# Optimization experiments

Hardware: AMD Instinct MI355X
Metric: run time of the kernel (lower is better)

The kernel has to match this reference:

```python
import jax, jax.numpy as jnp
import numpy as np

NC = 80          # num_classes
REG_MAX = 16
TOPK = 10
IMG = 640
STRIDES = (8, 16, 32)
EPS = 1e-9


def make_anchors(shapes, strides):
    pts, strs = [], []
    for (h, w), s in zip(shapes, strides):
        sx = jnp.arange(w, dtype=jnp.float32)  # grid_cell_offset = 0.0
        sy = jnp.arange(h, dtype=jnp.float32)
        gy, gx = jnp.meshgrid(sy, sx, indexing='ij')
        pts.append(jnp.stack([gx, gy], -1).reshape(-1, 2))
        strs.append(jnp.full((h * w, 1), float(s), dtype=jnp.float32))
    return jnp.concatenate(pts, 0), jnp.concatenate(strs, 0)  # [A,2], [A,1]


def ciou(box1, box2, eps=1e-7):
    # boxes are xyxy, broadcastable; returns CIoU with last dim squeezed
    b1x1, b1y1, b1x2, b1y2 = jnp.split(box1, 4, -1)
    b2x1, b2y1, b2x2, b2y2 = jnp.split(box2, 4, -1)
    w1, h1 = b1x2 - b1x1, b1y2 - b1y1
    w2, h2 = b2x2 - b2x1, b2y2 - b2y1
    inter = (jnp.clip(jnp.minimum(b1x2, b2x2) - jnp.maximum(b1x1, b2x1), 0.0)
             * jnp.clip(jnp.minimum(b1y2, b2y2) - jnp.maximum(b1y1, b2y1), 0.0))
    union = w1 * h1 + w2 * h2 - inter + eps
    iou = inter / union
    cw = jnp.maximum(b1x2, b2x2) - jnp.minimum(b1x1, b2x1)
    ch = jnp.maximum(b1y2, b2y2) - jnp.minimum(b1y1, b2y1)
    c2 = cw ** 2 + ch ** 2 + eps
    rho2 = ((b2x1 + b2x2 - b1x1 - b1x2) ** 2 + (b2y1 + b2y2 - b1y1 - b1y2) ** 2) / 4.0
    v = (4.0 / np.pi ** 2) * (jnp.arctan(w2 / (h2 + eps)) - jnp.arctan(w1 / (h1 + eps))) ** 2
    alpha = jax.lax.stop_gradient(v / (v - iou + (1.0 + eps)))
    return (iou - (rho2 / c2 + v * alpha))[..., 0]


def bbox_decode(anchor_points, pred_distri):
    # distribution-focal decode: softmax over REG_MAX bins, expectation, dist2bbox
    B, A, _ = pred_distri.shape
    pd = pred_distri.reshape(B, A, 4, REG_MAX)
    proj = jnp.arange(REG_MAX, dtype=jnp.float32)
    dist = jnp.einsum('bacr,r->bac', jax.nn.softmax(pd, -1), proj)  # [B,A,4] ltrb
    lt, rb = dist[..., :2], dist[..., 2:]
    return jnp.concatenate([anchor_points - lt, anchor_points + rb], -1)  # xyxy


def assigner(pd_scores, pd_bboxes, anc_points, gt_labels, gt_bboxes, mask_gt,
             alpha=0.5, beta=6.0):
    # pd_scores [B,A,C] (sigmoid), pd_bboxes [B,A,4], gt_* [B,M,...], mask_gt [B,M,1]
    B, A, C = pd_scores.shape
    M = gt_bboxes.shape[1]
    mask_gt = mask_gt.astype(jnp.float32)
    # anchors whose center lies inside each gt box
    lt = anc_points[None, None, :, :] - gt_bboxes[:, :, None, :2]   # [B,M,A,2]
    rb = gt_bboxes[:, :, None, 2:] - anc_points[None, None, :, :]
    mask_in_gts = (jnp.minimum(lt.min(-1), rb.min(-1)) > EPS).astype(jnp.float32)  # [B,M,A]
    mask = mask_in_gts * mask_gt
    # class score of each anchor at the gt's label
    sc = jnp.take_along_axis(pd_scores[:, None, :, :],
                             gt_labels[:, :, None, None].astype(jnp.int32), axis=-1)[..., 0]  # [B,M,A]
    overlaps = jnp.clip(ciou(gt_bboxes[:, :, None, :], pd_bboxes[:, None, :, :]), 0.0) * mask
    bbox_scores = sc * mask
    align_metric = (bbox_scores ** alpha) * (overlaps ** beta)  # [B,M,A]
    # top-k candidates per gt
    _, idxs = jax.lax.top_k(align_metric, TOPK)                 # [B,M,K]
    valid = jnp.broadcast_to(mask_gt > 0, (B, M, TOPK))
    idxs = jnp.where(valid, idxs, 0)
    cnt = jnp.zeros((B * M, A), jnp.float32).at[
        jnp.arange(B * M)[:, None], idxs.reshape(B * M, TOPK)
    ].add(valid.reshape(B * M, TOPK).astype(jnp.float32)).reshape(B, M, A)
    mask_topk = jnp.where(cnt > 1, 0.0, cnt)
    mask_pos = mask_topk * mask_in_gts * mask_gt               # [B,M,A]
    # resolve anchors assigned to multiple gts by max overlap
    fg = mask_pos.sum(1)                                       # [B,A]
    multi = fg[:, None, :] > 1
    is_max = jax.nn.one_hot(overlaps.argmax(1), M, dtype=jnp.float32).transpose(0, 2, 1)
    mask_pos = jnp.where(multi, is_max, mask_pos)
    fg_mask = mask_pos.sum(1)                                  # [B,A]
    tgt_idx = mask_pos.argmax(1)                               # [B,A]
    # gather targets
    flat = tgt_idx + jnp.arange(B)[:, None] * M
    t_labels = jnp.clip(gt_labels.reshape(-1)[flat], 0)        # [B,A]
    t_bboxes = gt_bboxes.reshape(-1, 4)[flat]                  # [B,A,4]
    t_scores = jax.nn.one_hot(t_labels, C, dtype=jnp.float32) * (fg_mask[..., None] > 0)
    # normalize scores by aligned metric
    am = align_metric * mask_pos
    pos_am = am.max(-1, keepdims=True)                         # [B,M,1]
    pos_ov = (overlaps * mask_pos).max(-1, keepdims=True)      # [B,M,1]
    norm = (am * pos_ov / (pos_am + EPS)).max(1)[..., None]    # [B,A,1]
    return t_bboxes, t_scores * norm, fg_mask > 0


def setup_inputs() -> dict:
    key = jax.random.key(0)
    ks = jax.random.split(key, 9)
    B, M = 16, 32
    inp = {
        'cls0': jax.random.normal(ks[0], (B, NC, 80, 80), jnp.float32),
        'cls1': jax.random.normal(ks[1], (B, NC, 40, 40), jnp.float32),
        'cls2': jax.random.normal(ks[2], (B, NC, 20, 20), jnp.float32),
        'reg0': jax.random.normal(ks[3], (B, 4 * REG_MAX, 80, 80), jnp.float32),
        'reg1': jax.random.normal(ks[4], (B, 4 * REG_MAX, 40, 40), jnp.float32),
        'reg2': jax.random.normal(ks[5], (B, 4 * REG_MAX, 20, 20), jnp.float32),
    }
    cxy = jax.random.uniform(ks[6], (B, M, 2), minval=0.1, maxval=0.9)
    wh = jax.random.uniform(ks[7], (B, M, 2), minval=0.02, maxval=0.25)
    inp['boxes'] = jnp.concatenate([cxy, wh], -1)  # normalized cxcywh
    inp['labels'] = jax.random.randint(ks[8], (B, M), 0, NC)
    return inp


def reference(cls0, cls1, cls2, reg0, reg1, reg2, boxes, labels):
    cls_out, reg_out = [cls0, cls1, cls2], [reg0, reg1, reg2]
    B = cls0.shape[0]
    anc, stride_t = make_anchors([r.shape[2:] for r in reg_out], STRIDES)
    pred_scores = jnp.concatenate(
        [c.transpose(0, 2, 3, 1).reshape(B, -1, NC) for c in cls_out], 1)        # [B,A,C]
    pred_distri = jnp.concatenate(
        [r.transpose(0, 2, 3, 1).reshape(B, -1, 4 * REG_MAX) for r in reg_out], 1)
    # gt2xyxy: normalized cxcywh -> pixel xyxy
    cx, cy, w, h = jnp.split(boxes, 4, -1)
    gt_bboxes = jnp.concatenate([(cx - w / 2) * IMG, (cy - h / 2) * IMG,
                                 (cx + w / 2) * IMG, (cy + h / 2) * IMG], -1)
    mask_gt = gt_bboxes.sum(2, keepdims=True) > 0.0
    pred_bboxes = bbox_decode(anc, pred_distri)                                   # anchor units
    sg = jax.lax.stop_gradient
    t_bboxes, t_scores, fg_mask = assigner(
        sg(jax.nn.sigmoid(pred_scores)), sg(pred_bboxes) * stride_t,
        anc * stride_t, labels, gt_bboxes, mask_gt)
    tss = jnp.maximum(t_scores.sum(), 1.0)
    # classification BCE-with-logits
    x, t = pred_scores, t_scores
    bce = jnp.maximum(x, 0.0) - x * t + jnp.log1p(jnp.exp(-jnp.abs(x)))
    l_cls = bce.sum() / tss
    # bbox CIoU loss
    t_bboxes = t_bboxes / stride_t
    weight = t_scores.sum(-1) * fg_mask                                           # [B,A]
    iou = ciou(pred_bboxes, t_bboxes)
    l_iou = ((1.0 - iou) * weight).sum() / tss
    # DFL loss
    tltrb = jnp.clip(jnp.concatenate([anc - t_bboxes[..., :2],
                                      t_bboxes[..., 2:] - anc], -1),
                     0.0, REG_MAX - 1 - 0.01)                                     # [B,A,4]
    logp = jax.nn.log_softmax(pred_distri.reshape(B, -1, 4, REG_MAX), -1)
    tl = jnp.floor(tltrb).astype(jnp.int32)
    wl = (tl + 1).astype(jnp.float32) - tltrb
    lp_tl = jnp.take_along_axis(logp, tl[..., None], -1)[..., 0]
    lp_tr = jnp.take_along_axis(logp, (tl + 1)[..., None], -1)[..., 0]
    dfl = (-(lp_tl * wl + lp_tr * (1.0 - wl))).mean(-1)                           # [B,A]
    l_dfl = (dfl * weight).sum() / tss
    loss = jnp.stack([0.5 * l_cls, 7.5 * l_iou, 1.5 * l_dfl])
    return loss.sum(), loss
```

## Files before the change

kernel.cpp:

```cpp
#include <hip/hip_runtime.h>

#define NB 16
#define NM 32
#define NA 8400
#define NCC 80
#define NREG 64
#define A0 6400
#define A1 1600
#define A2 400
#define CAP 768

#define TILES_PER_B 34
#define DEC_BLKS (NB * TILES_PER_B)
#define BCE_BLKS 2048
#define PRE_GRID (DEC_BLKS + BCE_BLKS)
#define PL_GRID 525


__device__ __forceinline__ void anch(int a, float& ax, float& ay, float& s, int& lvl, int& p) {
  if (a < A0)            { lvl = 0; p = a;          s = 8.f;  ax = (float)(p % 80); ay = (float)(p / 80); }
  else if (a < A0 + A1)  { lvl = 1; p = a - A0;     s = 16.f; ax = (float)(p % 40); ay = (float)(p / 40); }
  else                   { lvl = 2; p = a - A0 - A1; s = 32.f; ax = (float)(p % 20); ay = (float)(p / 20); }
}

__device__ __forceinline__ float cls_at(const float* c0, const float* c1, const float* c2,
                                        int b, int ch, int a) {
  if (a < A0)           return c0[((size_t)(b * NCC + ch)) * A0 + a];
  if (a < A0 + A1)      return c1[((size_t)(b * NCC + ch)) * A1 + (a - A0)];
  return c2[((size_t)(b * NCC + ch)) * A2 + (a - A0 - A1)];
}

__device__ __forceinline__ float reg_at(const float* r0, const float* r1, const float* r2,
                                        int b, int ch, int lvl, int p) {
  if (lvl == 0) return r0[((size_t)(b * NREG + ch)) * A0 + p];
  if (lvl == 1) return r1[((size_t)(b * NREG + ch)) * A1 + p];
  return r2[((size_t)(b * NREG + ch)) * A2 + p];
}

__device__ __forceinline__ void gtbox(const float* boxes, int b, int m,
                                      float& x1, float& y1, float& x2, float& y2, bool& valid) {
  const float* q = boxes + ((size_t)(b * NM + m)) * 4;
  float cx = q[0], cy = q[1], w = q[2], h = q[3];
  x1 = (cx - w * 0.5f) * 640.f; y1 = (cy - h * 0.5f) * 640.f;
  x2 = (cx + w * 0.5f) * 640.f; y2 = (cy + h * 0.5f) * 640.f;
  valid = (x1 + y1 + x2 + y2) > 0.f;
}

__device__ __forceinline__ float ciou_f(float b1x1, float b1y1, float b1x2, float b1y2,
                                        float b2x1, float b2y1, float b2x2, float b2y2) {
  const float eps = 1e-7f;
  float w1 = b1x2 - b1x1, h1 = b1y2 - b1y1;
  float w2 = b2x2 - b2x1, h2 = b2y2 - b2y1;
  float iw = fmaxf(fminf(b1x2, b2x2) - fmaxf(b1x1, b2x1), 0.f);
  float ih = fmaxf(fminf(b1y2, b2y2) - fmaxf(b1y1, b2y1), 0.f);
  float inter = iw * ih;
  float uni = w1 * h1 + w2 * h2 - inter + eps;
  float iou = inter / uni;
  float cw = fmaxf(b1x2, b2x2) - fminf(b1x1, b2x1);
  float ch = fmaxf(b1y2, b2y2) - fminf(b1y1, b2y1);
  float c2 = cw * cw + ch * ch + eps;
  float dx = b2x1 + b2x2 - b1x1 - b1x2;
  float dy = b2y1 + b2y2 - b1y1 - b1y2;
  float rho2 = (dx * dx + dy * dy) * 0.25f;
  float at = atanf(w2 / (h2 + eps)) - atanf(w1 / (h1 + eps));
  float v = 0.4052847345693511f * at * at;
  float alpha = v / (v - iou + (1.0f + eps));
  return iou - (rho2 / c2 + v * alpha);
}

__device__ __forceinline__ float align_of(float sc, float o) {
  float o2 = o * o, o4 = o2 * o2;
  return sqrtf(sc) * (o2 * o4);
}

__device__ __forceinline__ float softplus_fast(float x) {
  float e = __expf(-fabsf(x));
  return fmaxf(x, 0.f) + __logf(1.f + e);
}


__global__ __launch_bounds__(256) void k_pre3(
    const float* r0, const float* r1, const float* r2,
    const float* c0, const float* c1, const float* c2,
    float4* bb4, float4* mls4, int* fgcnt, int* msum,
    unsigned* pos_am, unsigned* pos_ov, double* gt_acc, double* bce_part) {
  __shared__ __align__(8) float lds[32 * 256];
  const int tid = threadIdx.x;

  if (blockIdx.x < DEC_BLKS) {
    const int d = blockIdx.x;
    const int b = d / TILES_PER_B, u = d % TILES_PER_B;
    int lvl, tile;
    if (u < 25)      { lvl = 0; tile = u; }
    else if (u < 32) { lvl = 1; tile = u - 25; }
    else             { lvl = 2; tile = u - 32; }
    const int HW   = (lvl == 0) ? A0 : (lvl == 1 ? A1 : A2);
    const int W    = (lvl == 0) ? 80 : (lvl == 1 ? 40 : 20);
    const int loff = (lvl == 0) ? 0  : (lvl == 1 ? A0 : A0 + A1);
    const float* rg = (lvl == 0) ? r0 : (lvl == 1 ? r1 : r2);
    const int base_p = tile * 256;
    const int valid  = min(256, HW - base_p);
    const float* src = rg + (size_t)b * NREG * HW + base_p;

    float dist[4], mlv[4];
#pragma unroll
    for (int ph = 0; ph < 2; ++ph) {
      for (int ch = 0; ch < 32; ++ch) {
        if (tid < valid)
          lds[ch * 256 + tid] = src[(size_t)(ph * 32 + ch) * HW + tid];
      }
      __syncthreads();
      if (tid < valid) {
#pragma unroll
        for (int sh = 0; sh < 2; ++sh) {
          const float* col = &lds[(sh * 16) * 256 + tid];
          float mx = col[0];
#pragma unroll
          for (int r = 1; r < 16; ++r) mx = fmaxf(mx, col[r * 256]);
          float se = 0.f, ws = 0.f;
#pragma unroll
          for (int r = 0; r < 16; ++r) {
            float e = __expf(col[r * 256] - mx);
            se += e; ws += e * (float)r;
          }
          dist[ph * 2 + sh] = ws / se;
          mlv[ph * 2 + sh]  = mx + __logf(se);
        }
      }
      __syncthreads();
    }
    if (tid < valid) {
      int p = base_p + tid;
      float ax = (float)(p % W), ay = (float)(p / W);
      int t = b * NA + loff + p;
      bb4[t]  = make_float4(ax - dist[0], ay - dist[1], ax + dist[2], ay + dist[3]);
      mls4[t] = make_float4(mlv[0], mlv[1], mlv[2], mlv[3]);
    }
  } else {
    const int bce_blk = blockIdx.x - DEC_BLKS;
    const int gz = bce_blk * 256 + tid;
    if (gz < NB * NA) { fgcnt[gz] = 0; msum[gz] = 0; }
    if (gz < NB * NM) { pos_am[gz] = 0u; pos_ov[gz] = 0u; }
    if (gz < NB * NM * 4) gt_acc[gz] = 0.0;

    const size_t N0 = (size_t)NB * NCC * A0 / 4;
    const size_t N1 = (size_t)NB * NCC * A1 / 4;
    const size_t N2 = (size_t)NB * NCC * A2 / 4;
    const size_t NT = N0 + N1 + N2;
    const float4* f0 = (const float4*)c0;
    const float4* f1 = (const float4*)c1;
    const float4* f2 = (const float4*)c2;
    const size_t i0 = (size_t)bce_blk * 256 + tid;
    const size_t stride = (size_t)BCE_BLKS * 256;
    float s0 = 0.f, s1 = 0.f;
    for (size_t i = i0; i < NT; i += stride) {
      float4 v;
      if (i < N0) v = f0[i];
      else if (i < N0 + N1) v = f1[i - N0];
      else v = f2[i - N0 - N1];
      s0 += softplus_fast(v.x) + softplus_fast(v.z);
      s1 += softplus_fast(v.y) + softplus_fast(v.w);
    }
    double* sred = (double*)lds;
    sred[tid] = (double)(s0 + s1);
    __syncthreads();
    for (int off = 128; off; off >>= 1) {
      if (tid < off) sred[tid] += sred[tid + off];
      __syncthreads();
    }
    if (tid == 0) bce_part[bce_blk] = sred[0];
  }
}


__global__ __launch_bounds__(256) void k_assign(
    const float* boxes, const int* labels, const float4* bb,
    const float* c0, const float* c1, const float* c2,
    int* fgcnt, int* msum) {
  __shared__ float sv[CAP];
  __shared__ int   si[CAP];
  __shared__ int   s_n;
  const int bm = blockIdx.x;
  const int b = bm / NM, m = bm % NM;
  const int tid = threadIdx.x;
  const int lane = tid & 63;

  float gx1, gy1, gx2, gy2; bool valid;
  gtbox(boxes, b, m, gx1, gy1, gx2, gy2, valid);
  if (!valid) return;
  int lbl = labels[bm]; if (lbl < 0) lbl = 0; if (lbl >= NCC) lbl = NCC - 1;
  if (tid == 0) s_n = 0;
  __syncthreads();

  const int   Ws[3]   = {80, 40, 20};
  const float ss[3]   = {8.f, 16.f, 32.f};
  const int   loff[3] = {0, A0, A0 + A1};
  int rx0[3], ry0[3], rw[3], bc[3];
  int total = 0;
  for (int l = 0; l < 3; ++l) {
    float s = ss[l]; int W = Ws[l];
    int ax0 = (int)floorf((gx1 + 1e-9f) / s);
    int ax1 = (int)ceilf((gx2 - 1e-9f) / s);
    int ay0 = (int)floorf((gy1 + 1e-9f) / s);
    int ay1 = (int)ceilf((gy2 - 1e-9f) / s);
    ax0 = max(ax0, 0); ay0 = max(ay0, 0);
    ax1 = min(ax1, W - 1); ay1 = min(ay1, W - 1);
    rx0[l] = ax0; ry0[l] = ay0;
    rw[l] = max(0, ax1 - ax0 + 1);
    int rhl = max(0, ay1 - ay0 + 1);
    bc[l] = total;
    total += rw[l] * rhl;
  }
  int iters = (total + 255) >> 8;
  for (int it = 0; it < iters; ++it) {
    int idx = it * 256 + tid;
    bool pred = false; float am = 0.f; int a = 0;
    if (idx < total) {
      int l = (idx >= bc[2]) ? 2 : ((idx >= bc[1]) ? 1 : 0);
      int r = idx - bc[l];
      int iy = r / rw[l], ix = r - iy * rw[l];
      int axg = rx0[l] + ix, ayg = ry0[l] + iy;
      a = loff[l] + ayg * Ws[l] + axg;
      float s = ss[l];
      float axp = (float)axg * s, ayp = (float)ayg * s;
      float mn = fminf(fminf(axp - gx1, ayp - gy1), fminf(gx2 - axp, gy2 - ayp));
      if (mn > 1e-9f) {
        pred = true;
        float4 pb = bb[(size_t)b * NA + a];
        float c = ciou_f(gx1, gy1, gx2, gy2, pb.x * s, pb.y * s, pb.z * s, pb.w * s);
        float o = fmaxf(c, 0.f);
        float x = cls_at(c0, c1, c2, b, lbl, a);
        float sc = 1.f / (1.f + expf(-x));
        am = align_of(sc, o);
      }
    }
    unsigned long long mask = __ballot(pred);
    if (mask) {
      int nact = __popcll(mask);
      int leader = __ffsll(mask) - 1;
      int basec = 0;
      if (lane == leader) basec = atomicAdd(&s_n, nact);
      basec = __shfl(basec, leader);
      if (pred) {
        int off = basec + __popcll(mask & ((1ull << lane) - 1ull));
        if (off < CAP) { sv[off] = am; si[off] = a; }
      }
    }
  }
  __syncthreads();
  int n = s_n; if (n > CAP) n = CAP;
  if (n == 0) return;
  if (tid >= 64) return;

  float v[12]; int ix[12];
#pragma unroll
  for (int k = 0; k < 12; ++k) {
    int j = k * 64 + tid;
    bool in = (j < n);
    v[k]  = in ? sv[j] : -2.f;
    ix[k] = in ? si[j] : (1 << 30);
  }
  int cnt = 0;
#pragma unroll
  for (int k = 0; k < 12; ++k) cnt += (v[k] > 0.f) ? 1 : 0;
  for (int o = 32; o; o >>= 1) cnt += __shfl_xor(cnt, o);
  int npos = cnt;

  if (npos > 10) {
    for (int p = 0; p < 10; ++p) {
      float bv = -1.f; int bi = 1 << 30;
#pragma unroll
      for (int k = 0; k < 12; ++k) {
        if (v[k] > bv || (v[k] == bv && ix[k] < bi)) { bv = v[k]; bi = ix[k]; }
      }
      for (int o = 32; o; o >>= 1) {
        float wv = __shfl_xor(bv, o); int wi = __shfl_xor(bi, o);
        if (wv > bv || (wv == bv && wi < bi)) { bv = wv; bi = wi; }
      }
#pragma unroll
      for (int k = 0; k < 12; ++k) if (ix[k] == bi) v[k] = -1.f;
      if (tid == 0) {
        atomicAdd(&fgcnt[(size_t)b * NA + bi], 1);
        atomicAdd(&msum[(size_t)b * NA + bi], m);
      }
    }
  } else {
#pragma unroll
    for (int k = 0; k < 12; ++k) {
      if (v[k] > 0.f) {
        atomicAdd(&fgcnt[(size_t)b * NA + ix[k]], 1);
        atomicAdd(&msum[(size_t)b * NA + ix[k]], m);
      }
    }
    int need = 10 - npos;
    for (int j = tid; j < n; j += 64) {
      if (sv[j] == 0.f) {
        int i = si[j];
        if (i < 10) {
          int pb = 0;
          for (int q = 0; q < n; ++q) pb += (sv[q] > 0.f && si[q] < i) ? 1 : 0;
          if (i - pb < need) {
            atomicAdd(&fgcnt[(size_t)b * NA + i], 1);
            atomicAdd(&msum[(size_t)b * NA + i], m);
          }
        }
      }
    }
  }
}


__global__ __launch_bounds__(256) void k_rp(
    const float* boxes, const int* labels,
    const float4* bb, const float4* mls,
    const float* c0, const float* c1, const float* c2,
    const float* r0, const float* r1, const float* r2,
    const int* fgcnt, const int* msum,
    unsigned* pos_am, unsigned* pos_ov, double* gt_acc) {
  int t = blockIdx.x * 256 + threadIdx.x;
  if (t >= NB * NA) return;
  int fg = fgcnt[t];
  if (fg == 0) return;
  int b = t / NA, a = t % NA;
  float ax, ay, s; int lvl, p;
  anch(a, ax, ay, s, lvl, p);
  float axp = ax * s, ayp = ay * s;
  float4 pb = bb[t];
  float px1 = pb.x * s, py1 = pb.y * s, px2 = pb.z * s, py2 = pb.w * s;
  int asn; float o;
  if (fg == 1) {
    asn = msum[t];
    float gx1, gy1, gx2, gy2; bool valid;
    gtbox(boxes, b, asn, gx1, gy1, gx2, gy2, valid);
    o = fmaxf(ciou_f(gx1, gy1, gx2, gy2, px1, py1, px2, py2), 0.f);
  } else {
    float bv = -1e30f; int bi = 0;
    for (int m = 0; m < NM; ++m) {
      float gx1, gy1, gx2, gy2; bool valid;
      gtbox(boxes, b, m, gx1, gy1, gx2, gy2, valid);
      float om = 0.f;
      if (valid) {
        float mn = fminf(fminf(axp - gx1, ayp - gy1), fminf(gx2 - axp, gy2 - ayp));
        if (mn > 1e-9f)
          om = fmaxf(ciou_f(gx1, gy1, gx2, gy2, px1, py1, px2, py2), 0.f);
      }
      if (om > bv) { bv = om; bi = m; }
    }
    asn = bi; o = bv;
  }
  if (o <= 0.f) return;
  int g = b * NM + asn;
  int lbl = labels[g]; if (lbl < 0) lbl = 0; if (lbl >= NCC) lbl = NCC - 1;
  float x = cls_at(c0, c1, c2, b, lbl, a);
  float sc = 1.f / (1.f + expf(-x));
  float am = align_of(sc, o);
  atomicMax(&pos_am[g], __float_as_uint(am));
  atomicMax(&pos_ov[g], __float_as_uint(o));
  if (am <= 0.f) return;

  float gx1, gy1, gx2, gy2; bool valid;
  gtbox(boxes, b, asn, gx1, gy1, gx2, gy2, valid);
  float inv_s = 1.f / s;
  float tx1 = gx1 * inv_s, ty1 = gy1 * inv_s, tx2 = gx2 * inv_s, ty2 = gy2 * inv_s;
  float iou = ciou_f(pb.x, pb.y, pb.z, pb.w, tx1, ty1, tx2, ty2);
  float4 ml = mls[t];
  float tgt[4] = { ax - tx1, ay - ty1, tx2 - ax, ty2 - ay };
  float mlv[4] = { ml.x, ml.y, ml.z, ml.w };
  float dfl = 0.f;
  for (int sd = 0; sd < 4; ++sd) {
    float tv = fminf(fmaxf(tgt[sd], 0.f), 14.99f);
    float tlf = floorf(tv);
    int tl = (int)tlf;
    float wl = (tlf + 1.f) - tv;
    float xtl = reg_at(r0, r1, r2, b, sd * 16 + tl,     lvl, p);
    float xtr = reg_at(r0, r1, r2, b, sd * 16 + tl + 1, lvl, p);
    dfl += -((xtl - mlv[sd]) * wl + (xtr - mlv[sd]) * (1.f - wl));
  }
  dfl *= 0.25f;
  atomicAdd(&gt_acc[g * 4 + 0], (double)am);
  atomicAdd(&gt_acc[g * 4 + 1], (double)(am * x));
  atomicAdd(&gt_acc[g * 4 + 2], (double)(am * (1.f - iou)));
  atomicAdd(&gt_acc[g * 4 + 3], (double)(am * dfl));
}


__global__ __launch_bounds__(256) void k_final(const double* bce_part, const double* gt_acc,
                                               const unsigned* pos_am, const unsigned* pos_ov,
                                               float* out) {
  const int tid = threadIdx.x;
  double tss = 0.0, sx = 0.0, siou = 0.0, sdfl = 0.0, bce = 0.0;
  for (int g = tid; g < NB * NM; g += 256) {
    float pam = __uint_as_float(pos_am[g]);
    float pov = __uint_as_float(pos_ov[g]);
    double sc = (double)pov / ((double)pam + 1e-9);
    tss  += gt_acc[g * 4 + 0] * sc;
    sx   += gt_acc[g * 4 + 1] * sc;
    siou += gt_acc[g * 4 + 2] * sc;
    sdfl += gt_acc[g * 4 + 3] * sc;
  }
  for (int i = tid; i < BCE_BLKS; i += 256) bce += bce_part[i];
  __shared__ double sred[256];
  double vals[5] = { tss, sx, siou, sdfl, bce };
  double tot[5];
  for (int q = 0; q < 5; ++q) {
    sred[tid] = vals[q];
    __syncthreads();
    for (int off = 128; off; off >>= 1) {
      if (tid < off) sred[tid] += sred[tid + off];
      __syncthreads();
    }
    tot[q] = sred[0];
    __syncthreads();
  }
  if (tid == 0) {
    double t = tot[0]; if (t < 1.0) t = 1.0;
    double l0 = 0.5 * (tot[4] - tot[1]) / t;
    double l1 = 7.5 * tot[2] / t;
    double l2 = 1.5 * tot[3] / t;
    out[0] = (float)(l0 + l1 + l2);
    out[1] = (float)l0;
    out[2] = (float)l1;
    out[3] = (float)l2;
  }
}


extern "C" void kernel_launch(void* const* d_in, const int* in_sizes, int n_in,
                              void* d_out, int out_size, void* d_ws, size_t ws_size,
                              hipStream_t stream) {
  (void)in_sizes; (void)n_in; (void)out_size; (void)ws_size;
  const float* cls0  = (const float*)d_in[0];
  const float* cls1  = (const float*)d_in[1];
  const float* cls2  = (const float*)d_in[2];
  const float* reg0  = (const float*)d_in[3];
  const float* reg1  = (const float*)d_in[4];
  const float* reg2  = (const float*)d_in[5];
  const float* boxes = (const float*)d_in[6];
  const int*   labels = (const int*)d_in[7];
  float* out = (float*)d_out;

  const size_t BA = (size_t)NB * NA;
  const int    BM = NB * NM;

  char* wsb = (char*)d_ws;
  double*   bce_part = (double*)wsb;
  double*   gt_acc   = bce_part + BCE_BLKS;
  unsigned* pos_am   = (unsigned*)(gt_acc + (size_t)BM * 4);
  unsigned* pos_ov   = pos_am + BM;
  int*      fgcnt    = (int*)(pos_ov + BM);
  int*      msum     = fgcnt + BA;
  float*    bbp      = (float*)(msum + BA);
  float*    mlsp     = bbp + BA * 4;

  float4* bb  = (float4*)bbp;
  float4* mls = (float4*)mlsp;

  k_pre3<<<PRE_GRID, 256, 0, stream>>>(reg0, reg1, reg2, cls0, cls1, cls2,
                                       bb, mls, fgcnt, msum, pos_am, pos_ov,
                                       gt_acc, bce_part);
  k_assign<<<BM, 256, 0, stream>>>(boxes, labels, (const float4*)bb,
                                   cls0, cls1, cls2, fgcnt, msum);
  k_rp<<<PL_GRID, 256, 0, stream>>>(boxes, labels, (const float4*)bb, (const float4*)mls,
                                    cls0, cls1, cls2, reg0, reg1, reg2,
                                    fgcnt, msum, pos_am, pos_ov, gt_acc);
  k_final<<<1, 256, 0, stream>>>(bce_part, gt_acc, pos_am, pos_ov, out);
}
```

Measured before the change: 64.58 us.

## Regroup kernels: BCE with assignment, fold final reduction into last block

The decode kernel now only decodes boxes and zeroes the workspace. The class-BCE reduction moves into the assignment kernel's grid, so its many blocks run alongside the 512 assignment blocks instead of alongside decode. The separate final-reduction kernel is removed: the per-anchor kernel ends with an atomic completion counter, and the last block to finish does the global reduction. This cuts one launch and improves GPU fill during assignment. The cost is a global atomic per block plus atomic reads to see other blocks' results.

```diff
diff --git a/kernel.cpp b/kernel.cpp
--- a/kernel.cpp
+++ b/kernel.cpp
@@ -12,8 +12,9 @@
 
 #define TILES_PER_B 34
 #define DEC_BLKS (NB * TILES_PER_B)
+#define ASN_BLKS (NB * NM)
 #define BCE_BLKS 2048
-#define PRE_GRID (DEC_BLKS + BCE_BLKS)
+#define MID_GRID (ASN_BLKS + BCE_BLKS)
 #define PL_GRID 525
 
 
@@ -79,70 +80,81 @@
 }
 
 
-__global__ __launch_bounds__(256) void k_pre3(
+__global__ __launch_bounds__(256) void k_dec(
     const float* r0, const float* r1, const float* r2,
+    float4* bb4, float4* mls4, int* fgcnt, int* msum,
+    unsigned* pos_am, unsigned* pos_ov, double* gt_acc, int* done_ctr) {
+  __shared__ float lds[32 * 256];
+  const int tid = threadIdx.x;
+  const int g = blockIdx.x * 256 + tid;
+  if (g < NB * NA) { fgcnt[g] = 0; msum[g] = 0; }
+  if (g < NB * NM) { pos_am[g] = 0u; pos_ov[g] = 0u; }
+  if (g < NB * NM * 4) gt_acc[g] = 0.0;
+  if (g == 0) *done_ctr = 0;
+
+  const int d = blockIdx.x;
+  const int b = d / TILES_PER_B, u = d % TILES_PER_B;
+  int lvl, tile;
+  if (u < 25)      { lvl = 0; tile = u; }
+  else if (u < 32) { lvl = 1; tile = u - 25; }
+  else             { lvl = 2; tile = u - 32; }
+  const int HW   = (lvl == 0) ? A0 : (lvl == 1 ? A1 : A2);
+  const int W    = (lvl == 0) ? 80 : (lvl == 1 ? 40 : 20);
+  const int loff = (lvl == 0) ? 0  : (lvl == 1 ? A0 : A0 + A1);
+  const float* rg = (lvl == 0) ? r0 : (lvl == 1 ? r1 : r2);
+  const int base_p = tile * 256;
+  const int valid  = min(256, HW - base_p);
+  const float* src = rg + (size_t)b * NREG * HW + base_p;
+
+  float dist[4], mlv[4];
+#pragma unroll
+  for (int ph = 0; ph < 2; ++ph) {
+    for (int ch = 0; ch < 32; ++ch) {
+      if (tid < valid)
+        lds[ch * 256 + tid] = src[(size_t)(ph * 32 + ch) * HW + tid];
+    }
+    __syncthreads();
+    if (tid < valid) {
+#pragma unroll
+      for (int sh = 0; sh < 2; ++sh) {
+        const float* col = &lds[(sh * 16) * 256 + tid];
+        float mx = col[0];
+#pragma unroll
+        for (int r = 1; r < 16; ++r) mx = fmaxf(mx, col[r * 256]);
+        float se = 0.f, ws = 0.f;
+#pragma unroll
+        for (int r = 0; r < 16; ++r) {
+          float e = __expf(col[r * 256] - mx);
+          se += e; ws += e * (float)r;
+        }
+        dist[ph * 2 + sh] = ws / se;
+        mlv[ph * 2 + sh]  = mx + __logf(se);
+      }
+    }
+    __syncthreads();
+  }
+  if (tid < valid) {
+    int p = base_p + tid;
+    float ax = (float)(p % W), ay = (float)(p / W);
+    int t = b * NA + loff + p;
+    bb4[t]  = make_float4(ax - dist[0], ay - dist[1], ax + dist[2], ay + dist[3]);
+    mls4[t] = make_float4(mlv[0], mlv[1], mlv[2], mlv[3]);
+  }
+}
+
+
+__global__ __launch_bounds__(256) void k_mid(
+    const float* boxes, const int* labels, const float4* bb,
     const float* c0, const float* c1, const float* c2,
-    float4* bb4, float4* mls4, int* fgcnt, int* msum,
-    unsigned* pos_am, unsigned* pos_ov, double* gt_acc, double* bce_part) {
-  __shared__ __align__(8) float lds[32 * 256];
+    int* fgcnt, int* msum, double* bce_part) {
+  __shared__ float sv[CAP];
+  __shared__ int   si[CAP];
+  __shared__ int   s_n;
+  __shared__ double sred[256];
   const int tid = threadIdx.x;
 
-  if (blockIdx.x < DEC_BLKS) {
-    const int d = blockIdx.x;
-    const int b = d / TILES_PER_B, u = d % TILES_PER_B;
-    int lvl, tile;
-    if (u < 25)      { lvl = 0; tile = u; }
-    else if (u < 32) { lvl = 1; tile = u - 25; }
-    else             { lvl = 2; tile = u - 32; }
-    const int HW   = (lvl == 0) ? A0 : (lvl == 1 ? A1 : A2);
-    const int W    = (lvl == 0) ? 80 : (lvl == 1 ? 40 : 20);
-    const int loff = (lvl == 0) ? 0  : (lvl == 1 ? A0 : A0 + A1);
-    const float* rg = (lvl == 0) ? r0 : (lvl == 1 ? r1 : r2);
-    const int base_p = tile * 256;
-    const int valid  = min(256, HW - base_p);
-    const float* src = rg + (size_t)b * NREG * HW + base_p;
-
-    float dist[4], mlv[4];
-#pragma unroll
-    for (int ph = 0; ph < 2; ++ph) {
-      for (int ch = 0; ch < 32; ++ch) {
-        if (tid < valid)
-          lds[ch * 256 + tid] = src[(size_t)(ph * 32 + ch) * HW + tid];
-      }
-      __syncthreads();
-      if (tid < valid) {
-#pragma unroll
-        for (int sh = 0; sh < 2; ++sh) {
-          const float* col = &lds[(sh * 16) * 256 + tid];
-          float mx = col[0];
-#pragma unroll
-          for (int r = 1; r < 16; ++r) mx = fmaxf(mx, col[r * 256]);
-          float se = 0.f, ws = 0.f;
-#pragma unroll
-          for (int r = 0; r < 16; ++r) {
-            float e = __expf(col[r * 256] - mx);
-            se += e; ws += e * (float)r;
-          }
-          dist[ph * 2 + sh] = ws / se;
-          mlv[ph * 2 + sh]  = mx + __logf(se);
-        }
-      }
-      __syncthreads();
-    }
-    if (tid < valid) {
-      int p = base_p + tid;
-      float ax = (float)(p % W), ay = (float)(p / W);
-      int t = b * NA + loff + p;
-      bb4[t]  = make_float4(ax - dist[0], ay - dist[1], ax + dist[2], ay + dist[3]);
-      mls4[t] = make_float4(mlv[0], mlv[1], mlv[2], mlv[3]);
-    }
-  } else {
-    const int bce_blk = blockIdx.x - DEC_BLKS;
-    const int gz = bce_blk * 256 + tid;
-    if (gz < NB * NA) { fgcnt[gz] = 0; msum[gz] = 0; }
-    if (gz < NB * NM) { pos_am[gz] = 0u; pos_ov[gz] = 0u; }
-    if (gz < NB * NM * 4) gt_acc[gz] = 0.0;
-
+  if (blockIdx.x >= ASN_BLKS) {
+    const int bce_blk = blockIdx.x - ASN_BLKS;
     const size_t N0 = (size_t)NB * NCC * A0 / 4;
     const size_t N1 = (size_t)NB * NCC * A1 / 4;
     const size_t N2 = (size_t)NB * NCC * A2 / 4;
@@ -161,7 +173,6 @@
       s0 += softplus_fast(v.x) + softplus_fast(v.z);
       s1 += softplus_fast(v.y) + softplus_fast(v.w);
     }
-    double* sred = (double*)lds;
     sred[tid] = (double)(s0 + s1);
     __syncthreads();
     for (int off = 128; off; off >>= 1) {
@@ -169,20 +180,11 @@
       __syncthreads();
     }
     if (tid == 0) bce_part[bce_blk] = sred[0];
-  }
-}
-
-
-__global__ __launch_bounds__(256) void k_assign(
-    const float* boxes, const int* labels, const float4* bb,
-    const float* c0, const float* c1, const float* c2,
-    int* fgcnt, int* msum) {
-  __shared__ float sv[CAP];
-  __shared__ int   si[CAP];
-  __shared__ int   s_n;
+    return;
+  }
+
   const int bm = blockIdx.x;
   const int b = bm / NM, m = bm % NM;
-  const int tid = threadIdx.x;
   const int lane = tid & 63;
 
   float gx1, gy1, gx2, gy2; bool valid;
@@ -310,93 +312,99 @@
 }
 
 
-__global__ __launch_bounds__(256) void k_rp(
+__global__ __launch_bounds__(256) void k_rpf(
     const float* boxes, const int* labels,
     const float4* bb, const float4* mls,
     const float* c0, const float* c1, const float* c2,
     const float* r0, const float* r1, const float* r2,
     const int* fgcnt, const int* msum,
-    unsigned* pos_am, unsigned* pos_ov, double* gt_acc) {
-  int t = blockIdx.x * 256 + threadIdx.x;
-  if (t >= NB * NA) return;
+    unsigned* pos_am, unsigned* pos_ov, double* gt_acc,
+    int* done_ctr, const double* bce_part, float* out) {
+  const int tid = threadIdx.x;
+  const int t = blockIdx.x * 256 + tid;
   int fg = fgcnt[t];
-  if (fg == 0) return;
-  int b = t / NA, a = t % NA;
-  float ax, ay, s; int lvl, p;
-  anch(a, ax, ay, s, lvl, p);
-  float axp = ax * s, ayp = ay * s;
-  float4 pb = bb[t];
-  float px1 = pb.x * s, py1 = pb.y * s, px2 = pb.z * s, py2 = pb.w * s;
-  int asn; float o;
-  if (fg == 1) {
-    asn = msum[t];
-    float gx1, gy1, gx2, gy2; bool valid;
-    gtbox(boxes, b, asn, gx1, gy1, gx2, gy2, valid);
-    o = fmaxf(ciou_f(gx1, gy1, gx2, gy2, px1, py1, px2, py2), 0.f);
-  } else {
-    float bv = -1e30f; int bi = 0;
-    for (int m = 0; m < NM; ++m) {
+  if (fg > 0) {
+    int b = t / NA, a = t % NA;
+    float ax, ay, s; int lvl, p;
+    anch(a, ax, ay, s, lvl, p);
+    float axp = ax * s, ayp = ay * s;
+    float4 pb = bb[t];
+    float px1 = pb.x * s, py1 = pb.y * s, px2 = pb.z * s, py2 = pb.w * s;
+    int asn; float o;
+    if (fg == 1) {
+      asn = msum[t];
       float gx1, gy1, gx2, gy2; bool valid;
-      gtbox(boxes, b, m, gx1, gy1, gx2, gy2, valid);
-      float om = 0.f;
-      if (valid) {
-        float mn = fminf(fminf(axp - gx1, ayp - gy1), fminf(gx2 - axp, gy2 - ayp));
-        if (mn > 1e-9f)
-          om = fmaxf(ciou_f(gx1, gy1, gx2, gy2, px1, py1, px2, py2), 0.f);
-      }
-      if (om > bv) { bv = om; bi = m; }
-    }
-    asn = bi; o = bv;
-  }
-  if (o <= 0.f) return;
-  int g = b * NM + asn;
-  int lbl = labels[g]; if (lbl < 0) lbl = 0; if (lbl >= NCC) lbl = NCC - 1;
-  float x = cls_at(c0, c1, c2, b, lbl, a);
-  float sc = 1.f / (1.f + expf(-x));
-  float am = align_of(sc, o);
-  atomicMax(&pos_am[g], __float_as_uint(am));
-  atomicMax(&pos_ov[g], __float_as_uint(o));
-  if (am <= 0.f) return;
-
-  float gx1, gy1, gx2, gy2; bool valid;
-  gtbox(boxes, b, asn, gx1, gy1, gx2, gy2, valid);
-  float inv_s = 1.f / s;
-  float tx1 = gx1 * inv_s, ty1 = gy1 * inv_s, tx2 = gx2 * inv_s, ty2 = gy2 * inv_s;
-  float iou = ciou_f(pb.x, pb.y, pb.z, pb.w, tx1, ty1, tx2, ty2);
-  float4 ml = mls[t];
-  float tgt[4] = { ax - tx1, ay - ty1, tx2 - ax, ty2 - ay };
-  float mlv[4] = { ml.x, ml.y, ml.z, ml.w };
-  float dfl = 0.f;
-  for (int sd = 0; sd < 4; ++sd) {
-    float tv = fminf(fmaxf(tgt[sd], 0.f), 14.99f);
-    float tlf = floorf(tv);
-    int tl = (int)tlf;
-    float wl = (tlf + 1.f) - tv;
-    float xtl = reg_at(r0, r1, r2, b, sd * 16 + tl,     lvl, p);
-    float xtr = reg_at(r0, r1, r2, b, sd * 16 + tl + 1, lvl, p);
-    dfl += -((xtl - mlv[sd]) * wl + (xtr - mlv[sd]) * (1.f - wl));
-  }
-  dfl *= 0.25f;
-  atomicAdd(&gt_acc[g * 4 + 0], (double)am);
-  atomicAdd(&gt_acc[g * 4 + 1], (double)(am * x));
-  atomicAdd(&gt_acc[g * 4 + 2], (double)(am * (1.f - iou)));
-  atomicAdd(&gt_acc[g * 4 + 3], (double)(am * dfl));
-}
-
-
-__global__ __launch_bounds__(256) void k_final(const double* bce_part, const double* gt_acc,
-                                               const unsigned* pos_am, const unsigned* pos_ov,
-                                               float* out) {
-  const int tid = threadIdx.x;
+      gtbox(boxes, b, asn, gx1, gy1, gx2, gy2, valid);
+      o = fmaxf(ciou_f(gx1, gy1, gx2, gy2, px1, py1, px2, py2), 0.f);
+    } else {
+      float bv = -1e30f; int bi = 0;
+      for (int m = 0; m < NM; ++m) {
+        float gx1, gy1, gx2, gy2; bool valid;
+        gtbox(boxes, b, m, gx1, gy1, gx2, gy2, valid);
+        float om = 0.f;
+        if (valid) {
+          float mn = fminf(fminf(axp - gx1, ayp - gy1), fminf(gx2 - axp, gy2 - ayp));
+          if (mn > 1e-9f)
+            om = fmaxf(ciou_f(gx1, gy1, gx2, gy2, px1, py1, px2, py2), 0.f);
+        }
+        if (om > bv) { bv = om; bi = m; }
+      }
+      asn = bi; o = bv;
+    }
+    if (o > 0.f) {
+      int g = b * NM + asn;
+      int lbl = labels[g]; if (lbl < 0) lbl = 0; if (lbl >= NCC) lbl = NCC - 1;
+      float x = cls_at(c0, c1, c2, b, lbl, a);
+      float sc = 1.f / (1.f + expf(-x));
+      float am = align_of(sc, o);
+      atomicMax(&pos_am[g], __float_as_uint(am));
+      atomicMax(&pos_ov[g], __float_as_uint(o));
+      if (am > 0.f) {
+        float gx1, gy1, gx2, gy2; bool valid;
+        gtbox(boxes, b, asn, gx1, gy1, gx2, gy2, valid);
+        float inv_s = 1.f / s;
+        float tx1 = gx1 * inv_s, ty1 = gy1 * inv_s, tx2 = gx2 * inv_s, ty2 = gy2 * inv_s;
+        float iou = ciou_f(pb.x, pb.y, pb.z, pb.w, tx1, ty1, tx2, ty2);
+        float4 ml = mls[t];
+        float tgt[4] = { ax - tx1, ay - ty1, tx2 - ax, ty2 - ay };
+        float mlv[4] = { ml.x, ml.y, ml.z, ml.w };
+        float dfl = 0.f;
+        for (int sd = 0; sd < 4; ++sd) {
+          float tv = fminf(fmaxf(tgt[sd], 0.f), 14.99f);
+          float tlf = floorf(tv);
+          int tl = (int)tlf;
+          float wl = (tlf + 1.f) - tv;
+          float xtl = reg_at(r0, r1, r2, b, sd * 16 + tl,     lvl, p);
+          float xtr = reg_at(r0, r1, r2, b, sd * 16 + tl + 1, lvl, p);
+          dfl += -((xtl - mlv[sd]) * wl + (xtr - mlv[sd]) * (1.f - wl));
+        }
+        dfl *= 0.25f;
+        atomicAdd(&gt_acc[g * 4 + 0], (double)am);
+        atomicAdd(&gt_acc[g * 4 + 1], (double)(am * x));
+        atomicAdd(&gt_acc[g * 4 + 2], (double)(am * (1.f - iou)));
+        atomicAdd(&gt_acc[g * 4 + 3], (double)(am * dfl));
+      }
+    }
+  }
+
+  __shared__ int s_last;
+  __syncthreads();
+  if (tid == 0) {
+    int old = atomicAdd(done_ctr, 1);
+    s_last = (old == (int)gridDim.x - 1) ? 1 : 0;
+  }
+  __syncthreads();
+  if (!s_last) return;
+
   double tss = 0.0, sx = 0.0, siou = 0.0, sdfl = 0.0, bce = 0.0;
   for (int g = tid; g < NB * NM; g += 256) {
-    float pam = __uint_as_float(pos_am[g]);
-    float pov = __uint_as_float(pos_ov[g]);
+    float pam = __uint_as_float(atomicAdd(&pos_am[g], 0u));
+    float pov = __uint_as_float(atomicAdd(&pos_ov[g], 0u));
     double sc = (double)pov / ((double)pam + 1e-9);
-    tss  += gt_acc[g * 4 + 0] * sc;
-    sx   += gt_acc[g * 4 + 1] * sc;
-    siou += gt_acc[g * 4 + 2] * sc;
-    sdfl += gt_acc[g * 4 + 3] * sc;
+    tss  += atomicAdd(&gt_acc[g * 4 + 0], 0.0) * sc;
+    sx   += atomicAdd(&gt_acc[g * 4 + 1], 0.0) * sc;
+    siou += atomicAdd(&gt_acc[g * 4 + 2], 0.0) * sc;
+    sdfl += atomicAdd(&gt_acc[g * 4 + 3], 0.0) * sc;
   }
   for (int i = tid; i < BCE_BLKS; i += 256) bce += bce_part[i];
   __shared__ double sred[256];
@@ -413,10 +421,10 @@
     __syncthreads();
   }
   if (tid == 0) {
-    double t = tot[0]; if (t < 1.0) t = 1.0;
-    double l0 = 0.5 * (tot[4] - tot[1]) / t;
-    double l1 = 7.5 * tot[2] / t;
-    double l2 = 1.5 * tot[3] / t;
+    double t5 = tot[0]; if (t5 < 1.0) t5 = 1.0;
+    double l0 = 0.5 * (tot[4] - tot[1]) / t5;
+    double l1 = 7.5 * tot[2] / t5;
+    double l2 = 1.5 * tot[3] / t5;
     out[0] = (float)(l0 + l1 + l2);
     out[1] = (float)l0;
     out[2] = (float)l1;
@@ -447,7 +455,8 @@
   double*   gt_acc   = bce_part + BCE_BLKS;
   unsigned* pos_am   = (unsigned*)(gt_acc + (size_t)BM * 4);
   unsigned* pos_ov   = pos_am + BM;
-  int*      fgcnt    = (int*)(pos_ov + BM);
+  int*      done_ctr = (int*)(pos_ov + BM);
+  int*      fgcnt    = done_ctr + 4;
   int*      msum     = fgcnt + BA;
   float*    bbp      = (float*)(msum + BA);
   float*    mlsp     = bbp + BA * 4;
@@ -455,13 +464,12 @@
   float4* bb  = (float4*)bbp;
   float4* mls = (float4*)mlsp;
 
-  k_pre3<<<PRE_GRID, 256, 0, stream>>>(reg0, reg1, reg2, cls0, cls1, cls2,
-                                       bb, mls, fgcnt, msum, pos_am, pos_ov,
-                                       gt_acc, bce_part);
-  k_assign<<<BM, 256, 0, stream>>>(boxes, labels, (const float4*)bb,
-                                   cls0, cls1, cls2, fgcnt, msum);
-  k_rp<<<PL_GRID, 256, 0, stream>>>(boxes, labels, (const float4*)bb, (const float4*)mls,
-                                    cls0, cls1, cls2, reg0, reg1, reg2,
-                                    fgcnt, msum, pos_am, pos_ov, gt_acc);
-  k_final<<<1, 256, 0, stream>>>(bce_part, gt_acc, pos_am, pos_ov, out);
-}
+  k_dec<<<DEC_BLKS, 256, 0, stream>>>(reg0, reg1, reg2, bb, mls,
+                                      fgcnt, msum, pos_am, pos_ov, gt_acc, done_ctr);
+  k_mid<<<MID_GRID, 256, 0, stream>>>(boxes, labels, (const float4*)bb,
+                                      cls0, cls1, cls2, fgcnt, msum, bce_part);
+  k_rpf<<<PL_GRID, 256, 0, stream>>>(boxes, labels, (const float4*)bb, (const float4*)mls,
+                                     cls0, cls1, cls2, reg0, reg1, reg2,
+                                     fgcnt, msum, pos_am, pos_ov, gt_acc,
+                                     done_ctr, bce_part, out);
+}
```

After: 58.62 us. 1.1x faster.
